# Kernel tuning notes

Hardware: AMD Instinct MI355X
Metric: run time of the kernel (lower is better)

## Reference

```python
import jax, jax.numpy as jnp
import numpy as np

CODEBOOK_SIZE = 4096
DIM = 64


def setup_inputs() -> dict:
    key = jax.random.key(0)
    kx, ke = jax.random.split(key)
    x = jax.random.normal(kx, (8, 4096, DIM), dtype=jnp.float32)
    embed = jax.random.normal(ke, (CODEBOOK_SIZE, DIM), dtype=jnp.float32)  # codebook [K, d]
    return {"x": x, "embed": embed}


def reference(x, embed):
    # Eval-mode forward of EuclideanCodebook (svq_temp=None -> argmax).
    shape = x.shape
    flatten = x.reshape(-1, shape[-1])            # [N, d]
    embed_sq = jnp.sum(embed * embed, axis=-1)    # [K]
    # dist = 2 * x @ embed.T - ||embed||^2  (negative squared distance up to a const in x)
    dist = 2.0 * jnp.matmul(flatten, embed.T) - embed_sq[None, :]  # [N, K]
    embed_ind = jnp.argmax(dist, axis=-1)         # [N]
    embed_ind = embed_ind.reshape(shape[:-1])     # [...]
    quantize = embed[embed_ind]                   # gather -> [..., d]
    return (quantize, embed_ind)
```

## Files before the change

### kernel.cpp

```cpp
#include <hip/hip_runtime.h>
#include <math.h>

#define N_ROWS 32768
#define K_CODES 4096
#define DIM 64
#define SPLITS 4
#define TILES_TOTAL (K_CODES / 32)
#define TILES_PER_SPLIT (TILES_TOTAL / SPLITS)
#define QUANT_ELEMS (N_ROWS * DIM)

typedef _Float16 half8 __attribute__((ext_vector_type(8)));
typedef float floatx16 __attribute__((ext_vector_type(16)));

__device__ __forceinline__ void gld16(const void* g, void* l) {
    __builtin_amdgcn_global_load_lds(
        (const __attribute__((address_space(1))) unsigned int*)g,
        (__attribute__((address_space(3))) unsigned int*)l, 16, 0, 0);
}

__global__ void prep_kernel(const float* __restrict__ embed,
                            float* __restrict__ sq, half8* __restrict__ ehi,
                            half8* __restrict__ elo) {
    __shared__ float part[256];
    const int tid = threadIdx.x;
    const int t = blockIdx.x * 256 + tid;
    const int l = t & 63;
    const int s = (t >> 6) & 3;
    const int c = blockIdx.x;
    const int col = l & 31;
    const int code = c * 32 + col;
    const int koff = (l >> 5) * 8 + 16 * s;
    const float* src = embed + (size_t)code * DIM + koff;
    half8 h, lo;
    float ss = 0.f;
#pragma unroll
    for (int j = 0; j < 8; ++j) {
        float v = src[j];
        ss = fmaf(v, v, ss);
        _Float16 hi = (_Float16)v;
        h[j] = hi;
        lo[j] = (_Float16)(v - (float)hi);
    }
    ehi[t] = h;
    elo[t] = lo;
    part[tid] = ss;
    __syncthreads();
    if (tid < 32) {
        float a = 0.f;
#pragma unroll
        for (int q = 0; q < 8; ++q) a += part[tid + 32 * (q & 1) + 64 * (q >> 1)];
        sq[c * 32 + tid] = a;
    }
}

__global__ __launch_bounds__(256, 4) void fused_dist_argmax32(
    const float* __restrict__ x, const float* __restrict__ sq,
    const half8* __restrict__ ehi, const half8* __restrict__ elo,
    float* __restrict__ pbest, int* __restrict__ pidx) {
    __shared__ char lbuf[8192];
    const int tid = threadIdx.x;
    const int lane = tid & 63;
    const int wave = tid >> 6;
    const int col = lane & 31;
    const int half_ = lane >> 5;
    const int row_base = blockIdx.x * 128 + wave * 32;
    const int split = blockIdx.y;
    const int c0 = split * TILES_PER_SPLIT;

    half8 ah[4], al[4];
    {
        const float* xs = x + (size_t)(row_base + col) * DIM + half_ * 8;
#pragma unroll
        for (int s = 0; s < 4; ++s) {
            half8 h, lo;
#pragma unroll
            for (int j = 0; j < 8; ++j) {
                float v = 2.0f * xs[16 * s + j];
                _Float16 hi = (_Float16)v;
                h[j] = hi;
                lo[j] = (_Float16)(v - (float)hi);
            }
            ah[s] = h;
            al[s] = lo;
        }
    }

    float best[16];
    int bidx[16];
#pragma unroll
    for (int r = 0; r < 16; ++r) {
        best[r] = -INFINITY;
        bidx[r] = 0;
    }

    const char* gh = (const char*)(ehi + (size_t)c0 * 256);
    const char* gl = (const char*)(elo + (size_t)c0 * 256);
    const float* psq = sq + c0 * 32 + col;
    const half8* lh = (const half8*)lbuf;
    const half8* ll = (const half8*)(lbuf + 4096);

    for (int c = 0; c < TILES_PER_SPLIT; ++c) {
        gld16(gh + (size_t)c * 4096 + (size_t)tid * 16, lbuf + tid * 16);
        gld16(gl + (size_t)c * 4096 + (size_t)tid * 16, lbuf + 4096 + tid * 16);
        float nsq = -psq[(size_t)c * 32];
        __syncthreads();

        floatx16 acc;
#pragma unroll
        for (int r = 0; r < 16; ++r) acc[r] = nsq;
        half8 b;
        b = lh[lane];
        acc = __builtin_amdgcn_mfma_f32_32x32x16_f16(ah[0], b, acc, 0, 0, 0);
        acc = __builtin_amdgcn_mfma_f32_32x32x16_f16(al[0], b, acc, 0, 0, 0);
        b = lh[64 + lane];
        acc = __builtin_amdgcn_mfma_f32_32x32x16_f16(ah[1], b, acc, 0, 0, 0);
        acc = __builtin_amdgcn_mfma_f32_32x32x16_f16(al[1], b, acc, 0, 0, 0);
        b = lh[128 + lane];
        acc = __builtin_amdgcn_mfma_f32_32x32x16_f16(ah[2], b, acc, 0, 0, 0);
        acc = __builtin_amdgcn_mfma_f32_32x32x16_f16(al[2], b, acc, 0, 0, 0);
        b = lh[192 + lane];
        acc = __builtin_amdgcn_mfma_f32_32x32x16_f16(ah[3], b, acc, 0, 0, 0);
        acc = __builtin_amdgcn_mfma_f32_32x32x16_f16(al[3], b, acc, 0, 0, 0);
        b = ll[lane];
        acc = __builtin_amdgcn_mfma_f32_32x32x16_f16(ah[0], b, acc, 0, 0, 0);
        b = ll[64 + lane];
        acc = __builtin_amdgcn_mfma_f32_32x32x16_f16(ah[1], b, acc, 0, 0, 0);
        b = ll[128 + lane];
        acc = __builtin_amdgcn_mfma_f32_32x32x16_f16(ah[2], b, acc, 0, 0, 0);
        b = ll[192 + lane];
        acc = __builtin_amdgcn_mfma_f32_32x32x16_f16(ah[3], b, acc, 0, 0, 0);
        __syncthreads();

        const int cidx = (c0 + c) * 32 + col;
#pragma unroll
        for (int r = 0; r < 16; ++r) {
            if (acc[r] > best[r]) {
                best[r] = acc[r];
                bidx[r] = cidx;
            }
        }
    }

#pragma unroll
    for (int r = 0; r < 16; ++r) {
        float bv = best[r];
        int bi = bidx[r];
#pragma unroll
        for (int d = 1; d < 32; d <<= 1) {
            float ov = __shfl_xor(bv, d);
            int oi = __shfl_xor(bi, d);
            if (ov > bv || (ov == bv && oi < bi)) {
                bv = ov;
                bi = oi;
            }
        }
        if (col == 0) {
            const int row = row_base + (r & 3) + 8 * (r >> 2) + 4 * half_;
            pbest[(size_t)split * N_ROWS + row] = bv;
            pidx[(size_t)split * N_ROWS + row] = bi;
        }
    }
}

__global__ void combine_kernel(const float* __restrict__ pbest,
                               const int* __restrict__ pidx,
                               const float* __restrict__ embed,
                               float* __restrict__ out) {
    const int t = blockIdx.x * blockDim.x + threadIdx.x;
    const int row = t >> 4;
    const int q = t & 15;
    if (row >= N_ROWS) return;

    float best = -INFINITY;
    int bi = 0;
#pragma unroll
    for (int s = 0; s < SPLITS; ++s) {
        float b = pbest[(size_t)s * N_ROWS + row];
        int i = pidx[(size_t)s * N_ROWS + row];
        if (b > best) {
            best = b;
            bi = i;
        }
    }

    const float4* e4 = reinterpret_cast<const float4*>(embed);
    float4 v = e4[(size_t)bi * (DIM / 4) + q];
    reinterpret_cast<float4*>(out)[(size_t)row * (DIM / 4) + q] = v;
    if (q == 0) {
        out[(size_t)QUANT_ELEMS + row] = (float)bi;
    }
}

extern "C" void kernel_launch(void* const* d_in, const int* in_sizes, int n_in,
                              void* d_out, int out_size, void* d_ws,
                              size_t ws_size, hipStream_t stream) {
    const float* x = (const float*)d_in[0];
    const float* embed = (const float*)d_in[1];
    float* out = (float*)d_out;

    char* ws = (char*)d_ws;
    float* sq = (float*)ws;
    half8* ehi = (half8*)(ws + 16384);
    half8* elo = (half8*)(ws + 16384 + 524288);
    float* pbest = (float*)(ws + 16384 + 2 * 524288);
    int* pidx = (int*)(ws + 16384 + 2 * 524288 + SPLITS * N_ROWS * 4);

    prep_kernel<<<TILES_TOTAL, 256, 0, stream>>>(embed, sq, ehi, elo);

    dim3 grid(N_ROWS / 128, SPLITS);
    fused_dist_argmax32<<<grid, 256, 0, stream>>>(x, sq, ehi, elo, pbest,
                                                  pidx);

    const int combine_threads = N_ROWS * (DIM / 4);
    combine_kernel<<<(combine_threads + 255) / 256, 256, 0, stream>>>(
        pbest, pidx, embed, out);
}
```

Before: 122.6 us.

## Fuse split argmax, combine and gather into one kernel with per-wave codebook splits

Replaces the split-K grid plus a separate combine kernel with one kernel. Each block handles 64 rows, and each of its four waves scans a quarter of the codebook, loading the fp16 hi/lo codebook tiles directly from global memory into registers instead of staging them through LDS with barriers. Each wave now computes two 32-row MFMA tiles per codebook tile, reusing the loaded B fragments across two accumulators. The cross-wave argmax reduction, index output and embedding gather happen in-block through shared memory, which removes the partial-result round trip and one launch. In exchange register pressure rises (launch bounds drop to 2) and every wave issues its own global loads with no cross-wave sharing.

```diff
diff --git a/kernel.cpp b/kernel.cpp
--- a/kernel.cpp
+++ b/kernel.cpp
@@ -4,19 +4,14 @@
 #define N_ROWS 32768
 #define K_CODES 4096
 #define DIM 64
-#define SPLITS 4
 #define TILES_TOTAL (K_CODES / 32)
-#define TILES_PER_SPLIT (TILES_TOTAL / SPLITS)
+#define TILES_PER_WAVE (TILES_TOTAL / 4)
 #define QUANT_ELEMS (N_ROWS * DIM)
 
 typedef _Float16 half8 __attribute__((ext_vector_type(8)));
 typedef float floatx16 __attribute__((ext_vector_type(16)));
 
-__device__ __forceinline__ void gld16(const void* g, void* l) {
-    __builtin_amdgcn_global_load_lds(
-        (const __attribute__((address_space(1))) unsigned int*)g,
-        (__attribute__((address_space(3))) unsigned int*)l, 16, 0, 0);
-}
+#define MFMA32(a, b, c) __builtin_amdgcn_mfma_f32_32x32x16_f16((a), (b), (c), 0, 0, 0)
 
 __global__ void prep_kernel(const float* __restrict__ embed,
                             float* __restrict__ sq, half8* __restrict__ ehi,
@@ -48,28 +43,32 @@
     if (tid < 32) {
         float a = 0.f;
 #pragma unroll
-        for (int q = 0; q < 8; ++q) a += part[tid + 32 * (q & 1) + 64 * (q >> 1)];
+        for (int q = 0; q < 8; ++q)
+            a += part[tid + 32 * (q & 1) + 64 * (q >> 1)];
         sq[c * 32 + tid] = a;
     }
 }
 
-__global__ __launch_bounds__(256, 4) void fused_dist_argmax32(
+__global__ __launch_bounds__(256, 2) void fused_all(
     const float* __restrict__ x, const float* __restrict__ sq,
     const half8* __restrict__ ehi, const half8* __restrict__ elo,
-    float* __restrict__ pbest, int* __restrict__ pidx) {
-    __shared__ char lbuf[8192];
+    const float* __restrict__ embed, float* __restrict__ out) {
+    __shared__ float rbest[4][64];
+    __shared__ int ridx[4][64];
+    __shared__ int fidx[64];
+
     const int tid = threadIdx.x;
     const int lane = tid & 63;
     const int wave = tid >> 6;
     const int col = lane & 31;
     const int half_ = lane >> 5;
-    const int row_base = blockIdx.x * 128 + wave * 32;
-    const int split = blockIdx.y;
-    const int c0 = split * TILES_PER_SPLIT;
-
-    half8 ah[4], al[4];
-    {
-        const float* xs = x + (size_t)(row_base + col) * DIM + half_ * 8;
+    const int row_base = blockIdx.x * 64;
+
+    half8 ah[2][4], al[2][4];
+#pragma unroll
+    for (int m = 0; m < 2; ++m) {
+        const float* xs =
+            x + (size_t)(row_base + m * 32 + col) * DIM + half_ * 8;
 #pragma unroll
         for (int s = 0; s < 4; ++s) {
             half8 h, lo;
@@ -80,71 +79,84 @@
                 h[j] = hi;
                 lo[j] = (_Float16)(v - (float)hi);
             }
-            ah[s] = h;
-            al[s] = lo;
-        }
-    }
-
-    float best[16];
-    int bidx[16];
+            ah[m][s] = h;
+            al[m][s] = lo;
+        }
+    }
+
+    float best0[16], best1[16];
+    int idx0[16], idx1[16];
 #pragma unroll
     for (int r = 0; r < 16; ++r) {
-        best[r] = -INFINITY;
-        bidx[r] = 0;
-    }
-
-    const char* gh = (const char*)(ehi + (size_t)c0 * 256);
-    const char* gl = (const char*)(elo + (size_t)c0 * 256);
+        best0[r] = -INFINITY;
+        best1[r] = -INFINITY;
+        idx0[r] = 0;
+        idx1[r] = 0;
+    }
+
+    const int c0 = wave * TILES_PER_WAVE;
+    const half8* ph = ehi + (size_t)c0 * 256 + lane;
+    const half8* pl = elo + (size_t)c0 * 256 + lane;
     const float* psq = sq + c0 * 32 + col;
-    const half8* lh = (const half8*)lbuf;
-    const half8* ll = (const half8*)(lbuf + 4096);
-
-    for (int c = 0; c < TILES_PER_SPLIT; ++c) {
-        gld16(gh + (size_t)c * 4096 + (size_t)tid * 16, lbuf + tid * 16);
-        gld16(gl + (size_t)c * 4096 + (size_t)tid * 16, lbuf + 4096 + tid * 16);
-        float nsq = -psq[(size_t)c * 32];
-        __syncthreads();
-
-        floatx16 acc;
-#pragma unroll
-        for (int r = 0; r < 16; ++r) acc[r] = nsq;
-        half8 b;
-        b = lh[lane];
-        acc = __builtin_amdgcn_mfma_f32_32x32x16_f16(ah[0], b, acc, 0, 0, 0);
-        acc = __builtin_amdgcn_mfma_f32_32x32x16_f16(al[0], b, acc, 0, 0, 0);
-        b = lh[64 + lane];
-        acc = __builtin_amdgcn_mfma_f32_32x32x16_f16(ah[1], b, acc, 0, 0, 0);
-        acc = __builtin_amdgcn_mfma_f32_32x32x16_f16(al[1], b, acc, 0, 0, 0);
-        b = lh[128 + lane];
-        acc = __builtin_amdgcn_mfma_f32_32x32x16_f16(ah[2], b, acc, 0, 0, 0);
-        acc = __builtin_amdgcn_mfma_f32_32x32x16_f16(al[2], b, acc, 0, 0, 0);
-        b = lh[192 + lane];
-        acc = __builtin_amdgcn_mfma_f32_32x32x16_f16(ah[3], b, acc, 0, 0, 0);
-        acc = __builtin_amdgcn_mfma_f32_32x32x16_f16(al[3], b, acc, 0, 0, 0);
-        b = ll[lane];
-        acc = __builtin_amdgcn_mfma_f32_32x32x16_f16(ah[0], b, acc, 0, 0, 0);
-        b = ll[64 + lane];
-        acc = __builtin_amdgcn_mfma_f32_32x32x16_f16(ah[1], b, acc, 0, 0, 0);
-        b = ll[128 + lane];
-        acc = __builtin_amdgcn_mfma_f32_32x32x16_f16(ah[2], b, acc, 0, 0, 0);
-        b = ll[192 + lane];
-        acc = __builtin_amdgcn_mfma_f32_32x32x16_f16(ah[3], b, acc, 0, 0, 0);
-        __syncthreads();
+
+    for (int c = 0; c < TILES_PER_WAVE; ++c) {
+        half8 bh0 = ph[0], bh1 = ph[64], bh2 = ph[128], bh3 = ph[192];
+        half8 bl0 = pl[0], bl1 = pl[64], bl2 = pl[128], bl3 = pl[192];
+        float nsq = -psq[0];
+        ph += 256;
+        pl += 256;
+        psq += 32;
+
+        floatx16 acc0, acc1;
+#pragma unroll
+        for (int r = 0; r < 16; ++r) {
+            acc0[r] = nsq;
+            acc1[r] = nsq;
+        }
+        acc0 = MFMA32(ah[0][0], bh0, acc0);
+        acc1 = MFMA32(ah[1][0], bh0, acc1);
+        acc0 = MFMA32(al[0][0], bh0, acc0);
+        acc1 = MFMA32(al[1][0], bh0, acc1);
+        acc0 = MFMA32(ah[0][0], bl0, acc0);
+        acc1 = MFMA32(ah[1][0], bl0, acc1);
+        acc0 = MFMA32(ah[0][1], bh1, acc0);
+        acc1 = MFMA32(ah[1][1], bh1, acc1);
+        acc0 = MFMA32(al[0][1], bh1, acc0);
+        acc1 = MFMA32(al[1][1], bh1, acc1);
+        acc0 = MFMA32(ah[0][1], bl1, acc0);
+        acc1 = MFMA32(ah[1][1], bl1, acc1);
+        acc0 = MFMA32(ah[0][2], bh2, acc0);
+        acc1 = MFMA32(ah[1][2], bh2, acc1);
+        acc0 = MFMA32(al[0][2], bh2, acc0);
+        acc1 = MFMA32(al[1][2], bh2, acc1);
+        acc0 = MFMA32(ah[0][2], bl2, acc0);
+        acc1 = MFMA32(ah[1][2], bl2, acc1);
+        acc0 = MFMA32(ah[0][3], bh3, acc0);
+        acc1 = MFMA32(ah[1][3], bh3, acc1);
+        acc0 = MFMA32(al[0][3], bh3, acc0);
+        acc1 = MFMA32(al[1][3], bh3, acc1);
+        acc0 = MFMA32(ah[0][3], bl3, acc0);
+        acc1 = MFMA32(ah[1][3], bl3, acc1);
 
         const int cidx = (c0 + c) * 32 + col;
 #pragma unroll
         for (int r = 0; r < 16; ++r) {
-            if (acc[r] > best[r]) {
-                best[r] = acc[r];
-                bidx[r] = cidx;
+            if (acc0[r] > best0[r]) {
+                best0[r] = acc0[r];
+                idx0[r] = cidx;
+            }
+            if (acc1[r] > best1[r]) {
+                best1[r] = acc1[r];
+                idx1[r] = cidx;
             }
         }
     }
 
 #pragma unroll
     for (int r = 0; r < 16; ++r) {
-        float bv = best[r];
-        int bi = bidx[r];
+        const int row = (r & 3) + 8 * (r >> 2) + 4 * half_;
+        float bv = best0[r];
+        int bi = idx0[r];
 #pragma unroll
         for (int d = 1; d < 32; d <<= 1) {
             float ov = __shfl_xor(bv, d);
@@ -155,39 +167,53 @@
             }
         }
         if (col == 0) {
-            const int row = row_base + (r & 3) + 8 * (r >> 2) + 4 * half_;
-            pbest[(size_t)split * N_ROWS + row] = bv;
-            pidx[(size_t)split * N_ROWS + row] = bi;
-        }
-    }
-}
-
-__global__ void combine_kernel(const float* __restrict__ pbest,
-                               const int* __restrict__ pidx,
-                               const float* __restrict__ embed,
-                               float* __restrict__ out) {
-    const int t = blockIdx.x * blockDim.x + threadIdx.x;
-    const int row = t >> 4;
-    const int q = t & 15;
-    if (row >= N_ROWS) return;
-
-    float best = -INFINITY;
-    int bi = 0;
-#pragma unroll
-    for (int s = 0; s < SPLITS; ++s) {
-        float b = pbest[(size_t)s * N_ROWS + row];
-        int i = pidx[(size_t)s * N_ROWS + row];
-        if (b > best) {
-            best = b;
-            bi = i;
-        }
-    }
-
+            rbest[wave][row] = bv;
+            ridx[wave][row] = bi;
+        }
+        bv = best1[r];
+        bi = idx1[r];
+#pragma unroll
+        for (int d = 1; d < 32; d <<= 1) {
+            float ov = __shfl_xor(bv, d);
+            int oi = __shfl_xor(bi, d);
+            if (ov > bv || (ov == bv && oi < bi)) {
+                bv = ov;
+                bi = oi;
+            }
+        }
+        if (col == 0) {
+            rbest[wave][row + 32] = bv;
+            ridx[wave][row + 32] = bi;
+        }
+    }
+    __syncthreads();
+
+    if (tid < 64) {
+        float bv = rbest[0][tid];
+        int bi = ridx[0][tid];
+#pragma unroll
+        for (int w = 1; w < 4; ++w) {
+            float b = rbest[w][tid];
+            if (b > bv) {
+                bv = b;
+                bi = ridx[w][tid];
+            }
+        }
+        fidx[tid] = bi;
+        out[(size_t)QUANT_ELEMS + row_base + tid] = (float)bi;
+    }
+    __syncthreads();
+
+    const int grow = tid >> 2;
+    const int q0 = tid & 3;
+    const int bi = fidx[grow];
     const float4* e4 = reinterpret_cast<const float4*>(embed);
-    float4 v = e4[(size_t)bi * (DIM / 4) + q];
-    reinterpret_cast<float4*>(out)[(size_t)row * (DIM / 4) + q] = v;
-    if (q == 0) {
-        out[(size_t)QUANT_ELEMS + row] = (float)bi;
+    float4* o4 = reinterpret_cast<float4*>(out);
+#pragma unroll
+    for (int q = 0; q < 4; ++q) {
+        const int chunk = q0 + 4 * q;
+        o4[(size_t)(row_base + grow) * (DIM / 4) + chunk] =
+            e4[(size_t)bi * (DIM / 4) + chunk];
     }
 }
 
@@ -202,16 +228,8 @@
     float* sq = (float*)ws;
     half8* ehi = (half8*)(ws + 16384);
     half8* elo = (half8*)(ws + 16384 + 524288);
-    float* pbest = (float*)(ws + 16384 + 2 * 524288);
-    int* pidx = (int*)(ws + 16384 + 2 * 524288 + SPLITS * N_ROWS * 4);
 
     prep_kernel<<<TILES_TOTAL, 256, 0, stream>>>(embed, sq, ehi, elo);
 
-    dim3 grid(N_ROWS / 128, SPLITS);
-    fused_dist_argmax32<<<grid, 256, 0, stream>>>(x, sq, ehi, elo, pbest,
-                                                  pidx);
-
-    const int combine_threads = N_ROWS * (DIM / 4);
-    combine_kernel<<<(combine_threads + 255) / 256, 256, 0, stream>>>(
-        pbest, pidx, embed, out);
+    fused_all<<<N_ROWS / 64, 256, 0, stream>>>(x, sq, ehi, elo, embed, out);
 }
```

Measured after the change: 128.2 us. 1.05x slower.
